# Kernel optimization log

Hardware: AMD Instinct MI355X
Metric: run time of the kernel (lower is better)

## Reference

```python
import jax, jax.numpy as jnp
import numpy as np
import math

D_QKV = 64


def setup_inputs() -> dict:
    key = jax.random.key(0)
    ks = jax.random.split(key, 6)
    b, l, d_model, n_head, d_qkv = 2, 2048, 1024, 16, D_QKV
    return {
        "x": jax.random.normal(ks[0], (b, l, d_model), dtype=jnp.float32),
        "w_q": jax.random.normal(ks[1], (n_head, d_model, d_qkv), dtype=jnp.float32) * (2.0 / (d_model + d_qkv)) ** 0.5,
        "w_k": jax.random.normal(ks[2], (n_head, d_model, d_qkv), dtype=jnp.float32) * (2.0 / (d_model + d_qkv)) ** 0.5,
        "w_v": jax.random.normal(ks[3], (n_head, d_model, d_qkv), dtype=jnp.float32) * (2.0 / (d_model + d_qkv)) ** 0.5,
        "w_o": jax.random.normal(ks[4], (n_head, d_qkv, d_model), dtype=jnp.float32) * (2.0 / (d_model + d_qkv)) ** 0.5,
        "mask": jnp.zeros((b, 1, 1, l), dtype=bool),  # True = masked (padding)
    }


def reference(x, w_q, w_k, w_v, w_o, mask):
    # x: [b, l, m]; w_{q,k,v}: [n, m, d]; w_o: [n, d, m]; mask broadcastable to [b, n, l, l]
    q = jnp.einsum("blm,nmd->bnld", x, w_q)
    k = jnp.einsum("blm,nmd->bnld", x, w_k)
    v = jnp.einsum("blm,nmd->bnld", x, w_v)
    scores = jnp.einsum("bnld,bnkd->bnlk", q, k) / math.sqrt(D_QKV)
    scores = jnp.where(mask, jnp.float32(-1e9), scores)
    attn = jax.nn.softmax(scores, axis=-1)  # dropout is identity (p=0 / eval)
    ctx = jnp.einsum("bnlk,bnkd->bnld", attn, v)
    # per-head output projection then sum over heads: V.matmul(w_o).sum(dim=1)
    return jnp.einsum("bnld,ndm->blm", ctx, w_o)
```

## Files before the change

kernel.cpp:

```cpp
#include <hip/hip_runtime.h>
#include <stdint.h>

using bf16x8  = __attribute__((ext_vector_type(8))) short;
using f32x4   = __attribute__((ext_vector_type(4))) float;
using f32x16  = __attribute__((ext_vector_type(16))) float;
using ushort8 = __attribute__((ext_vector_type(8))) unsigned short;
using ushort4v= __attribute__((ext_vector_type(4))) unsigned short;
using uint2v  = __attribute__((ext_vector_type(2))) unsigned int;

typedef __attribute__((address_space(1))) const unsigned int* gas_ptr;
typedef __attribute__((address_space(3))) unsigned int*       las_ptr;

__device__ __forceinline__ void gload_lds16(const unsigned short* g, unsigned short* l) {
    __builtin_amdgcn_global_load_lds((gas_ptr)(const void*)g, (las_ptr)(void*)l, 16, 0, 0);
}

__device__ __forceinline__ unsigned short f2bf(float f) {
    union { float f; uint32_t u; } x; x.f = f;
    uint32_t u = x.u;
    uint32_t r = u + 0x7fffu + ((u >> 16) & 1u);
    return (unsigned short)(r >> 16);
}
__device__ __forceinline__ float bf2f(unsigned short u) {
    union { uint32_t u; float f; } x; x.u = ((uint32_t)u) << 16;
    return x.f;
}

__device__ __forceinline__ f32x4 mfma16(bf16x8 a, bf16x8 b, f32x4 c) {
    return __builtin_amdgcn_mfma_f32_16x16x32_bf16(a, b, c, 0, 0, 0);
}
__device__ __forceinline__ f32x16 mfma32(bf16x8 a, bf16x8 b, f32x16 c) {
    return __builtin_amdgcn_mfma_f32_32x32x16_bf16(a, b, c, 0, 0, 0);
}

__device__ __forceinline__ unsigned int cvtpk_bf16(float lo, float hi) {
    unsigned int r;
    asm("v_cvt_pk_bf16_f32 %0, %1, %2" : "=v"(r) : "v"(lo), "v"(hi));
    return r;
}
__device__ __forceinline__ void plswap(unsigned int& a, unsigned int& b) {
    asm("v_permlane32_swap_b32 %0, %1" : "+v"(a), "+v"(b));
}


__global__ void cast_x_kernel(const float* __restrict__ x, unsigned short* __restrict__ xb) {
    int i = blockIdx.x * 256 + threadIdx.x;
    using f32x4v = __attribute__((ext_vector_type(4))) float;
    f32x4v v = ((const f32x4v*)x)[i];
    ushort4v o;
    o[0] = f2bf(v[0]); o[1] = f2bf(v[1]); o[2] = f2bf(v[2]); o[3] = f2bf(v[3]);
    ((ushort4v*)xb)[i] = o;
}

__global__ void pack_wqkv_t(const float* __restrict__ wq, const float* __restrict__ wk,
                            const float* __restrict__ wv, unsigned short* __restrict__ wpT) {
    __shared__ float tile[64][65];
    const int mm = blockIdx.y;
    const int s = mm >> 4, hh = mm & 15;
    const float* src = ((s == 0) ? wq : (s == 1) ? wk : wv) + (size_t)hh * 1024 * 64;
    const int k0 = blockIdx.x * 64;
    const int c = threadIdx.x & 63, rg = threadIdx.x >> 6;
#pragma unroll
    for (int i = 0; i < 16; ++i) {
        int r = rg * 16 + i;
        tile[r][c] = src[(size_t)(k0 + r) * 64 + c];
    }
    __syncthreads();
    unsigned short* dst = wpT + ((size_t)s * 1024 + hh * 64) * 1024 + k0;
    const int kc = threadIdx.x & 63, dg = threadIdx.x >> 6;
#pragma unroll
    for (int i = 0; i < 16; ++i) {
        int d = dg * 16 + i;
        dst[(size_t)d * 1024 + kc] = f2bf(tile[kc][d]);
    }
}

__global__ void pack_wo_t(const float* __restrict__ wo, unsigned short* __restrict__ woT) {
    __shared__ float tile[64][65];
    const int r0 = blockIdx.y * 64;
    const int c0 = blockIdx.x * 64;
    const int c = threadIdx.x & 63, rg = threadIdx.x >> 6;
#pragma unroll
    for (int i = 0; i < 16; ++i) {
        int r = rg * 16 + i;
        tile[r][c] = wo[(size_t)(r0 + r) * 1024 + c0 + c];
    }
    __syncthreads();
    const int kc = threadIdx.x & 63, mg = threadIdx.x >> 6;
#pragma unroll
    for (int i = 0; i < 16; ++i) {
        int m = mg * 16 + i;
        woT[(size_t)(c0 + m) * 1024 + r0 + kc] = f2bf(tile[kc][m]);
    }
}


template<int MODE, int BN>
__global__ __launch_bounds__(256) void gemm_bt(
    const unsigned short* __restrict__ A,
    const unsigned short* __restrict__ BT,
    float* __restrict__ Cf,
    unsigned short* __restrict__ Q,
    unsigned short* __restrict__ Kq,
    unsigned short* __restrict__ V,
    int M, int N, int K)
{
    constexpr int NF = BN / 32;
    __shared__ unsigned short As[128 * 64];
    __shared__ unsigned short Bs[BN * 64];
    const int tid  = threadIdx.x;
    const int lane = tid & 63;
    const int wave = tid >> 6;
    const int wm = wave >> 1, wn = wave & 1;
    const int l15 = lane & 15, l4 = lane >> 4;
    const int row0 = blockIdx.y * 128;
    const int col0 = blockIdx.x * BN;

    f32x4 acc[4][NF];
#pragma unroll
    for (int i = 0; i < 4; ++i)
#pragma unroll
        for (int j = 0; j < NF; ++j) acc[i][j] = (f32x4){0.f, 0.f, 0.f, 0.f};

    for (int k0 = 0; k0 < K; k0 += 64) {
        __syncthreads();
#pragma unroll
        for (int it = 0; it < 4; ++it) {
            int cb = (it * 4 + wave) * 64;
            int c  = cb + lane;
            int r  = c >> 3, c8 = c & 7;
            int sc8 = c8 ^ (r & 7);
            gload_lds16(&A[(size_t)(row0 + r) * K + k0 + sc8 * 8], &As[cb * 8]);
        }
#pragma unroll
        for (int it = 0; it < NF; ++it) {
            int cb = (it * 4 + wave) * 64;
            int c  = cb + lane;
            int r  = c >> 3, c8 = c & 7;
            int sc8 = c8 ^ (r & 7);
            gload_lds16(&BT[(size_t)(col0 + r) * K + k0 + sc8 * 8], &Bs[cb * 8]);
        }
        __syncthreads();
#pragma unroll
        for (int kk = 0; kk < 2; ++kk) {
            bf16x8 af[4], bfr[NF];
#pragma unroll
            for (int m = 0; m < 4; ++m) {
                int r   = wm * 64 + m * 16 + l15;
                int blk = (kk * 4 + l4) ^ (r & 7);
                af[m] = *(const bf16x8*)&As[r * 64 + blk * 8];
            }
#pragma unroll
            for (int n = 0; n < NF; ++n) {
                int r   = wn * (BN / 2) + n * 16 + l15;
                int blk = (kk * 4 + l4) ^ (r & 7);
                bfr[n] = *(const bf16x8*)&Bs[r * 64 + blk * 8];
            }
#pragma unroll
            for (int m = 0; m < 4; ++m)
#pragma unroll
                for (int n = 0; n < NF; ++n)
                    acc[m][n] = mfma16(af[m], bfr[n], acc[m][n]);
        }
    }

#pragma unroll
    for (int m = 0; m < 4; ++m) {
#pragma unroll
        for (int n = 0; n < NF; ++n) {
#pragma unroll
            for (int r = 0; r < 4; ++r) {
                int gr = row0 + wm * 64 + m * 16 + l4 * 4 + r;
                int gc = col0 + wn * (BN / 2) + n * 16 + l15;
                float v = acc[m][n][r];
                if (MODE == 0) {
                    int s = gc >> 10, rem = gc & 1023;
                    int hh = rem >> 6, dd = rem & 63;
                    int bb = gr >> 11, ll = gr & 2047;
                    unsigned short* dst = (s == 0) ? Q : (s == 1) ? Kq : V;
                    dst[(((size_t)bb * 16 + hh) * 2048 + ll) * 64 + dd] = f2bf(v);
                } else {
                    Cf[(size_t)gr * N + gc] = v;
                }
            }
        }
    }
}


template<int SPLIT>
__global__ __launch_bounds__(256) void attn_kernel(
    const unsigned short* __restrict__ qb,
    const unsigned short* __restrict__ kb,
    const unsigned short* __restrict__ vb,
    const unsigned char* __restrict__ mask,
    unsigned short* __restrict__ ctxb,
    unsigned short* __restrict__ part,
    float* __restrict__ ml)
{
    const int lg = blockIdx.x;
    int qt, h, b, t0;
    int half = 0;
    if (SPLIT) {
        int u = ((lg & 7) << 7) | (lg >> 3);
        int bh = u >> 5, sub = u & 31;
        qt = sub >> 1; half = sub & 1;
        b = bh >> 4; h = bh & 15;
        t0 = half * 16;
    } else {
        int swz = ((lg & 7) << 6) | (lg >> 3);
        qt = swz & 15; h = (swz >> 4) & 15; b = swz >> 8; t0 = 0;
    }
    const int NT = SPLIT ? 16 : 32;

    const int tid  = threadIdx.x;
    const int lane = tid & 63, wave = tid >> 6;
    const int l31  = lane & 31, hi = lane >> 5;

    __shared__ unsigned short smem[16384];
    __shared__ int flags[32];

    const size_t hoff = ((size_t)(b * 16 + h)) * 2048 * 64;
    const unsigned short* qh = qb + hoff;
    const unsigned short* kh = kb + hoff;
    const unsigned short* vh = vb + hoff;
    const unsigned char*  mb = mask + (size_t)b * 2048;

    if (tid < 32) flags[tid] = 0;
    __syncthreads();
    {
        uint2v mv = *(const uint2v*)&mb[tid * 8];
        if (mv[0] | mv[1]) flags[tid >> 3] = 1;
    }

    const int qrow = qt * 128 + wave * 32 + l31;
    bf16x8 qf[4];
#pragma unroll
    for (int ki = 0; ki < 4; ++ki)
        qf[ki] = *(const bf16x8*)&qh[(size_t)qrow * 64 + ki * 16 + hi * 8];

    f32x16 accA = {0,0,0,0,0,0,0,0,0,0,0,0,0,0,0,0};
    f32x16 accB = {0,0,0,0,0,0,0,0,0,0,0,0,0,0,0,0};
    float m_r = -1e30f, l_r = 0.f;
    const float SC  = 0.18033688011112042f;
    const float THR = 44.3614195558365f;

    const int krow = tid >> 3, kc16 = tid & 7;
    const int vd = tid & 63, vcb = (tid >> 6) * 2;

    ushort8 kreg[2];
    unsigned short vreg[16];
    {
        const int kvb = t0 * 64;
#pragma unroll
        for (int it = 0; it < 2; ++it)
            kreg[it] = *(const ushort8*)&kh[(size_t)(kvb + krow + it * 32) * 64 + kc16 * 8];
#pragma unroll
        for (int j = 0; j < 16; ++j)
            vreg[j] = vh[(size_t)(kvb + vcb * 8 + j) * 64 + vd];
    }

    for (int t = t0; t < t0 + NT; ++t) {
        const int kv0 = t * 64;
        unsigned short* Kb = smem + (t & 1) * 4096;
        unsigned short* Vb = smem + 8192 + (t & 1) * 4096;

#pragma unroll
        for (int it = 0; it < 2; ++it) {
            int r = krow + it * 32;
            *(ushort8*)&Kb[r * 64 + ((kc16 ^ (r & 7)) * 8)] = kreg[it];
        }
        {
            union { unsigned short u[16]; ushort8 v[2]; } p;
#pragma unroll
            for (int j = 0; j < 16; ++j) p.u[j] = vreg[j];
#pragma unroll
            for (int c = 0; c < 2; ++c) {
                int cc = vcb + c;
                *(ushort8*)&Vb[vd * 64 + ((cc ^ (vd & 7)) * 8)] = p.v[c];
            }
        }
        __syncthreads();

        if (t < t0 + NT - 1) {
            const int kvn = kv0 + 64;
#pragma unroll
            for (int it = 0; it < 2; ++it)
                kreg[it] = *(const ushort8*)&kh[(size_t)(kvn + krow + it * 32) * 64 + kc16 * 8];
#pragma unroll
            for (int j = 0; j < 16; ++j)
                vreg[j] = vh[(size_t)(kvn + vcb * 8 + j) * 64 + vd];
        }

        f32x16 s0 = {0,0,0,0,0,0,0,0,0,0,0,0,0,0,0,0};
        f32x16 s1 = {0,0,0,0,0,0,0,0,0,0,0,0,0,0,0,0};
        __builtin_amdgcn_s_setprio(1);
#pragma unroll
        for (int ki = 0; ki < 4; ++ki) {
            int c0 = ((ki * 2 + hi) ^ (l31 & 7)) * 8;
            bf16x8 a0 = *(const bf16x8*)&Kb[l31 * 64 + c0];
            bf16x8 a1 = *(const bf16x8*)&Kb[(32 + l31) * 64 + c0];
            s0 = mfma32(a0, qf[ki], s0);
            s1 = mfma32(a1, qf[ki], s1);
        }
        __builtin_amdgcn_s_setprio(0);

        if (flags[t]) {
#pragma unroll
            for (int r = 0; r < 16; ++r) {
                int keyl = (r & 3) + 8 * (r >> 2) + 4 * hi;
                if (mb[kv0 + keyl])      s0[r] = -1e30f;
                if (mb[kv0 + 32 + keyl]) s1[r] = -1e30f;
            }
        }

        float mx;
        {
            float a0 = fmaxf(fmaxf(s0[0], s0[1]),  fmaxf(s0[2],  s0[3]));
            float a1 = fmaxf(fmaxf(s0[4], s0[5]),  fmaxf(s0[6],  s0[7]));
            float a2 = fmaxf(fmaxf(s0[8], s0[9]),  fmaxf(s0[10], s0[11]));
            float a3 = fmaxf(fmaxf(s0[12], s0[13]), fmaxf(s0[14], s0[15]));
            float b0 = fmaxf(fmaxf(s1[0], s1[1]),  fmaxf(s1[2],  s1[3]));
            float b1 = fmaxf(fmaxf(s1[4], s1[5]),  fmaxf(s1[6],  s1[7]));
            float b2 = fmaxf(fmaxf(s1[8], s1[9]),  fmaxf(s1[10], s1[11]));
            float b3 = fmaxf(fmaxf(s1[12], s1[13]), fmaxf(s1[14], s1[15]));
            mx = fmaxf(fmaxf(fmaxf(a0, a1), fmaxf(a2, a3)),
                       fmaxf(fmaxf(b0, b1), fmaxf(b2, b3)));
        }
        mx = fmaxf(mx, __shfl_xor(mx, 32));
        if (__any(mx > m_r + THR)) {
            float mn  = fmaxf(m_r, mx);
            float scl = __builtin_amdgcn_exp2f((m_r - mn) * SC);
            m_r = mn;
            l_r *= scl;
#pragma unroll
            for (int i = 0; i < 16; ++i) { accA[i] *= scl; accB[i] *= scl; }
        }
        const float nmc = -m_r * SC;
#pragma unroll
        for (int i = 0; i < 16; ++i) {
            s0[i] = __builtin_amdgcn_exp2f(__builtin_fmaf(s0[i], SC, nmc));
            s1[i] = __builtin_amdgcn_exp2f(__builtin_fmaf(s1[i], SC, nmc));
        }
        float rs;
        {
            float a0 = (s0[0] + s0[1]) + (s0[2] + s0[3]);
            float a1 = (s0[4] + s0[5]) + (s0[6] + s0[7]);
            float a2 = (s0[8] + s0[9]) + (s0[10] + s0[11]);
            float a3 = (s0[12] + s0[13]) + (s0[14] + s0[15]);
            float b0 = (s1[0] + s1[1]) + (s1[2] + s1[3]);
            float b1 = (s1[4] + s1[5]) + (s1[6] + s1[7]);
            float b2 = (s1[8] + s1[9]) + (s1[10] + s1[11]);
            float b3 = (s1[12] + s1[13]) + (s1[14] + s1[15]);
            rs = ((a0 + a1) + (a2 + a3)) + ((b0 + b1) + (b2 + b3));
        }
        rs += __shfl_xor(rs, 32);
        l_r += rs;

        bf16x8 pf[4];
        {
            union { unsigned int u[4]; bf16x8 v; } f;
            unsigned int w0 = cvtpk_bf16(s0[0],  s0[1]),  w1 = cvtpk_bf16(s0[2],  s0[3]);
            unsigned int w2 = cvtpk_bf16(s0[4],  s0[5]),  w3 = cvtpk_bf16(s0[6],  s0[7]);
            unsigned int w4 = cvtpk_bf16(s0[8],  s0[9]),  w5 = cvtpk_bf16(s0[10], s0[11]);
            unsigned int w6 = cvtpk_bf16(s0[12], s0[13]), w7 = cvtpk_bf16(s0[14], s0[15]);
            plswap(w0, w2); plswap(w1, w3); plswap(w4, w6); plswap(w5, w7);
            f.u[0] = w0; f.u[1] = w1; f.u[2] = w2; f.u[3] = w3; pf[0] = f.v;
            f.u[0] = w4; f.u[1] = w5; f.u[2] = w6; f.u[3] = w7; pf[1] = f.v;
            unsigned int x0 = cvtpk_bf16(s1[0],  s1[1]),  x1 = cvtpk_bf16(s1[2],  s1[3]);
            unsigned int x2 = cvtpk_bf16(s1[4],  s1[5]),  x3 = cvtpk_bf16(s1[6],  s1[7]);
            unsigned int x4 = cvtpk_bf16(s1[8],  s1[9]),  x5 = cvtpk_bf16(s1[10], s1[11]);
            unsigned int x6 = cvtpk_bf16(s1[12], s1[13]), x7 = cvtpk_bf16(s1[14], s1[15]);
            plswap(x0, x2); plswap(x1, x3); plswap(x4, x6); plswap(x5, x7);
            f.u[0] = x0; f.u[1] = x1; f.u[2] = x2; f.u[3] = x3; pf[2] = f.v;
            f.u[0] = x4; f.u[1] = x5; f.u[2] = x6; f.u[3] = x7; pf[3] = f.v;
        }

        __builtin_amdgcn_s_setprio(1);
#pragma unroll
        for (int ks = 0; ks < 4; ++ks) {
            int c0 = ((ks * 2 + hi) ^ (l31 & 7)) * 8;
            bf16x8 vA = *(const bf16x8*)&Vb[l31 * 64 + c0];
            bf16x8 vB = *(const bf16x8*)&Vb[(32 + l31) * 64 + c0];
            accA = mfma32(vA, pf[ks], accA);
            accB = mfma32(vB, pf[ks], accB);
        }
        __builtin_amdgcn_s_setprio(0);
    }

    __syncthreads();
    const int qloc = wave * 32 + l31;
    const float inv = SPLIT ? 1.0f : (1.0f / l_r);
#pragma unroll
    for (int r = 0; r < 16; ++r) {
        int dA = (r & 3) + 8 * (r >> 2) + 4 * hi;
        smem[qloc * 64 + (dA ^ ((qloc & 7) * 8))]        = f2bf(accA[r] * inv);
        smem[qloc * 64 + ((32 + dA) ^ ((qloc & 7) * 8))] = f2bf(accB[r] * inv);
    }
    if (SPLIT && hi == 0) {
        size_t mrow = ((size_t)half * 32 + b * 16 + h) * 2048 + qt * 128 + qloc;
        *(float2*)&ml[mrow * 2] = make_float2(m_r, l_r);
    }
    __syncthreads();
    if (SPLIT) {
        const size_t prow0 = ((size_t)half * 32 + (b * 16 + h)) * 2048 + qt * 128;
#pragma unroll
        for (int it = 0; it < 4; ++it) {
            int idx = tid + it * 256;
            int q = idx >> 3, c = idx & 7;
            ushort8 vv = *(const ushort8*)&smem[q * 64 + ((c * 8) ^ ((q & 7) * 8))];
            *(ushort8*)&part[(prow0 + q) * 64 + c * 8] = vv;
        }
    } else {
#pragma unroll
        for (int it = 0; it < 4; ++it) {
            int idx = tid + it * 256;
            int q = idx >> 3, c = idx & 7;
            ushort8 vv = *(const ushort8*)&smem[q * 64 + ((c * 8) ^ ((q & 7) * 8))];
            *(ushort8*)&ctxb[((size_t)(b * 2048 + qt * 128 + q)) * 1024 + h * 64 + c * 8] = vv;
        }
    }
}


__global__ void combine_kernel(const unsigned short* __restrict__ part,
                               const float* __restrict__ ml,
                               unsigned short* __restrict__ ctxb)
{
    const float SC = 0.18033688011112042f;
    int gid = blockIdx.x * 256 + threadIdx.x;
    int row = gid >> 6, d = gid & 63;
    float p0 = bf2f(part[(size_t)row * 64 + d]);
    float p1 = bf2f(part[(size_t)(65536 + row) * 64 + d]);
    float2 a = *(const float2*)&ml[(size_t)row * 2];
    float2 c = *(const float2*)&ml[(size_t)(65536 + row) * 2];
    float m  = fmaxf(a.x, c.x);
    float w0 = __builtin_amdgcn_exp2f((a.x - m) * SC);
    float w1 = __builtin_amdgcn_exp2f((c.x - m) * SC);
    float l  = a.y * w0 + c.y * w1;
    float o  = (p0 * w0 + p1 * w1) / l;
    int bh = row >> 11, ql = row & 2047;
    int bb = bh >> 4, hh = bh & 15;
    ctxb[((size_t)(bb * 2048 + ql)) * 1024 + hh * 64 + d] = f2bf(o);
}


extern "C" void kernel_launch(void* const* d_in, const int* in_sizes, int n_in,
                              void* d_out, int out_size, void* d_ws, size_t ws_size,
                              hipStream_t stream)
{
    const float* x  = (const float*)d_in[0];
    const float* wq = (const float*)d_in[1];
    const float* wk = (const float*)d_in[2];
    const float* wv = (const float*)d_in[3];
    const float* wo = (const float*)d_in[4];
    const unsigned char* mask = (const unsigned char*)d_in[5];
    float* out = (float*)d_out;

    char* ws = (char*)d_ws;
    unsigned short* xb   = (unsigned short*)(ws);
    unsigned short* wpT  = (unsigned short*)(ws + 8388608);
    unsigned short* woT  = (unsigned short*)(ws + 14680064);
    unsigned short* qb   = (unsigned short*)(ws + 16777216);
    unsigned short* kb   = (unsigned short*)(ws + 25165824);
    unsigned short* vb   = (unsigned short*)(ws + 33554432);
    unsigned short* ctxb = (unsigned short*)(ws + 41943040);
    unsigned short* part = (unsigned short*)(ws + 50331648);
    float*          mlb  = (float*)(ws + 67108864);
    const bool split = ws_size >= (size_t)68157440;

    cast_x_kernel<<<4096, 256, 0, stream>>>(x, xb);
    pack_wqkv_t  <<<dim3(16, 48), 256, 0, stream>>>(wq, wk, wv, wpT);
    pack_wo_t    <<<dim3(16, 16), 256, 0, stream>>>(wo, woT);

    gemm_bt<0,128><<<dim3(24, 32), 256, 0, stream>>>(xb, wpT, nullptr, qb, kb, vb, 4096, 3072, 1024);

    if (split) {
        attn_kernel<1><<<1024, 256, 0, stream>>>(qb, kb, vb, mask, nullptr, part, mlb);
        combine_kernel<<<16384, 256, 0, stream>>>(part, mlb, ctxb);
    } else {
        attn_kernel<0><<<512, 256, 0, stream>>>(qb, kb, vb, mask, ctxb, nullptr, nullptr);
    }

    gemm_bt<1,64><<<dim3(16, 32), 256, 0, stream>>>(ctxb, woT, out, nullptr, nullptr, nullptr, 4096, 1024, 1024);
}
```

Before: 139.1 us.

## Always use split-KV attention by aliasing scratch onto dead buffers; vectorize combine

The split-KV attention path previously ran only when the workspace was large enough, and otherwise fell back to a 512-block, non-split kernel. It is now always used. The two partial outputs and the max/sum buffer are placed in the cast-x buffer, which is dead after the QKV GEMM, and in the output buffer, which the final projection GEMM overwrites anyway. This doubles the attention grid to 1024 blocks for better load balance across CUs. The combine kernel now handles 8 bf16 values per thread with vector loads and stores and a single reciprocal, at the cost of an extra combine pass and partial-output traffic.

```diff
diff --git a/kernel.cpp b/kernel.cpp
--- a/kernel.cpp
+++ b/kernel.cpp
@@ -188,30 +188,22 @@
 }
 
 
-template<int SPLIT>
 __global__ __launch_bounds__(256) void attn_kernel(
     const unsigned short* __restrict__ qb,
     const unsigned short* __restrict__ kb,
     const unsigned short* __restrict__ vb,
     const unsigned char* __restrict__ mask,
-    unsigned short* __restrict__ ctxb,
-    unsigned short* __restrict__ part,
+    unsigned short* __restrict__ part0,
+    unsigned short* __restrict__ part1,
     float* __restrict__ ml)
 {
     const int lg = blockIdx.x;
-    int qt, h, b, t0;
-    int half = 0;
-    if (SPLIT) {
-        int u = ((lg & 7) << 7) | (lg >> 3);
-        int bh = u >> 5, sub = u & 31;
-        qt = sub >> 1; half = sub & 1;
-        b = bh >> 4; h = bh & 15;
-        t0 = half * 16;
-    } else {
-        int swz = ((lg & 7) << 6) | (lg >> 3);
-        qt = swz & 15; h = (swz >> 4) & 15; b = swz >> 8; t0 = 0;
-    }
-    const int NT = SPLIT ? 16 : 32;
+    int u = ((lg & 7) << 7) | (lg >> 3);
+    int bh = u >> 5, sub = u & 31;
+    const int qt = sub >> 1, half = sub & 1;
+    const int b = bh >> 4, h = bh & 15;
+    const int t0 = half * 16;
+    const int NT = 16;
 
     const int tid  = threadIdx.x;
     const int lane = tid & 63, wave = tid >> 6;
@@ -390,58 +382,52 @@
 
     __syncthreads();
     const int qloc = wave * 32 + l31;
-    const float inv = SPLIT ? 1.0f : (1.0f / l_r);
 #pragma unroll
     for (int r = 0; r < 16; ++r) {
         int dA = (r & 3) + 8 * (r >> 2) + 4 * hi;
-        smem[qloc * 64 + (dA ^ ((qloc & 7) * 8))]        = f2bf(accA[r] * inv);
-        smem[qloc * 64 + ((32 + dA) ^ ((qloc & 7) * 8))] = f2bf(accB[r] * inv);
-    }
-    if (SPLIT && hi == 0) {
+        smem[qloc * 64 + (dA ^ ((qloc & 7) * 8))]        = f2bf(accA[r]);
+        smem[qloc * 64 + ((32 + dA) ^ ((qloc & 7) * 8))] = f2bf(accB[r]);
+    }
+    if (hi == 0) {
         size_t mrow = ((size_t)half * 32 + b * 16 + h) * 2048 + qt * 128 + qloc;
         *(float2*)&ml[mrow * 2] = make_float2(m_r, l_r);
     }
     __syncthreads();
-    if (SPLIT) {
-        const size_t prow0 = ((size_t)half * 32 + (b * 16 + h)) * 2048 + qt * 128;
-#pragma unroll
-        for (int it = 0; it < 4; ++it) {
-            int idx = tid + it * 256;
-            int q = idx >> 3, c = idx & 7;
-            ushort8 vv = *(const ushort8*)&smem[q * 64 + ((c * 8) ^ ((q & 7) * 8))];
-            *(ushort8*)&part[(prow0 + q) * 64 + c * 8] = vv;
-        }
-    } else {
-#pragma unroll
-        for (int it = 0; it < 4; ++it) {
-            int idx = tid + it * 256;
-            int q = idx >> 3, c = idx & 7;
-            ushort8 vv = *(const ushort8*)&smem[q * 64 + ((c * 8) ^ ((q & 7) * 8))];
-            *(ushort8*)&ctxb[((size_t)(b * 2048 + qt * 128 + q)) * 1024 + h * 64 + c * 8] = vv;
-        }
-    }
-}
-
-
-__global__ void combine_kernel(const unsigned short* __restrict__ part,
+    unsigned short* pdst = half ? part1 : part0;
+    const size_t prow0 = ((size_t)(b * 16 + h)) * 2048 + qt * 128;
+#pragma unroll
+    for (int it = 0; it < 4; ++it) {
+        int idx = tid + it * 256;
+        int q = idx >> 3, c = idx & 7;
+        ushort8 vv = *(const ushort8*)&smem[q * 64 + ((c * 8) ^ ((q & 7) * 8))];
+        *(ushort8*)&pdst[(prow0 + q) * 64 + c * 8] = vv;
+    }
+}
+
+
+__global__ void combine_kernel(const unsigned short* __restrict__ part0,
+                               const unsigned short* __restrict__ part1,
                                const float* __restrict__ ml,
                                unsigned short* __restrict__ ctxb)
 {
     const float SC = 0.18033688011112042f;
     int gid = blockIdx.x * 256 + threadIdx.x;
-    int row = gid >> 6, d = gid & 63;
-    float p0 = bf2f(part[(size_t)row * 64 + d]);
-    float p1 = bf2f(part[(size_t)(65536 + row) * 64 + d]);
+    int row = gid >> 3, c = gid & 7;
+    ushort8 v0 = *(const ushort8*)&part0[(size_t)row * 64 + c * 8];
+    ushort8 v1 = *(const ushort8*)&part1[(size_t)row * 64 + c * 8];
     float2 a = *(const float2*)&ml[(size_t)row * 2];
-    float2 c = *(const float2*)&ml[(size_t)(65536 + row) * 2];
-    float m  = fmaxf(a.x, c.x);
+    float2 d = *(const float2*)&ml[(size_t)(65536 + row) * 2];
+    float m  = fmaxf(a.x, d.x);
     float w0 = __builtin_amdgcn_exp2f((a.x - m) * SC);
-    float w1 = __builtin_amdgcn_exp2f((c.x - m) * SC);
-    float l  = a.y * w0 + c.y * w1;
-    float o  = (p0 * w0 + p1 * w1) / l;
+    float w1 = __builtin_amdgcn_exp2f((d.x - m) * SC);
+    float li = 1.0f / (a.y * w0 + d.y * w1);
+    ushort8 o;
+#pragma unroll
+    for (int j = 0; j < 8; ++j)
+        o[j] = f2bf((bf2f(v0[j]) * w0 + bf2f(v1[j]) * w1) * li);
     int bh = row >> 11, ql = row & 2047;
     int bb = bh >> 4, hh = bh & 15;
-    ctxb[((size_t)(bb * 2048 + ql)) * 1024 + hh * 64 + d] = f2bf(o);
+    *(ushort8*)&ctxb[((size_t)(bb * 2048 + ql)) * 1024 + hh * 64 + c * 8] = o;
 }
 
 
@@ -465,9 +451,9 @@
     unsigned short* kb   = (unsigned short*)(ws + 25165824);
     unsigned short* vb   = (unsigned short*)(ws + 33554432);
     unsigned short* ctxb = (unsigned short*)(ws + 41943040);
-    unsigned short* part = (unsigned short*)(ws + 50331648);
-    float*          mlb  = (float*)(ws + 67108864);
-    const bool split = ws_size >= (size_t)68157440;
+    unsigned short* part0 = xb;
+    unsigned short* part1 = (unsigned short*)d_out;
+    float*          mlb   = (float*)((char*)d_out + 8388608);
 
     cast_x_kernel<<<4096, 256, 0, stream>>>(x, xb);
     pack_wqkv_t  <<<dim3(16, 48), 256, 0, stream>>>(wq, wk, wv, wpT);
@@ -475,12 +461,8 @@
 
     gemm_bt<0,128><<<dim3(24, 32), 256, 0, stream>>>(xb, wpT, nullptr, qb, kb, vb, 4096, 3072, 1024);
 
-    if (split) {
-        attn_kernel<1><<<1024, 256, 0, stream>>>(qb, kb, vb, mask, nullptr, part, mlb);
-        combine_kernel<<<16384, 256, 0, stream>>>(part, mlb, ctxb);
-    } else {
-        attn_kernel<0><<<512, 256, 0, stream>>>(qb, kb, vb, mask, ctxb, nullptr, nullptr);
-    }
+    attn_kernel<<<1024, 256, 0, stream>>>(qb, kb, vb, mask, part0, part1, mlb);
+    combine_kernel<<<2048, 256, 0, stream>>>(part0, part1, mlb, ctxb);
 
     gemm_bt<1,64><<<dim3(16, 32), 256, 0, stream>>>(ctxb, woT, out, nullptr, nullptr, nullptr, 4096, 1024, 1024);
 }
```

Result: faster. 135.6 us (-2.5%).
